# Kernel optimization log

Hardware: AMD Instinct MI355X
Metric: run time of the kernel (lower is better)

Reference implementation:

```python
import jax, jax.numpy as jnp
import numpy as np

ROUTINGS = 3

def squash(s, axis=-1):
    mag_sq = jnp.sum(s * s, axis=axis, keepdims=True)
    mag = jnp.sqrt(mag_sq)
    return mag_sq / (1.0 + mag_sq) * (s / (mag + 1e-8))

def setup_inputs() -> dict:
    key = jax.random.key(0)
    k1, k2 = jax.random.split(key)
    B, I, Din, O, Dout = 256, 1152, 8, 10, 16
    x = jax.random.normal(k1, (B, I, Din), dtype=jnp.float32)
    weight = 0.01 * jax.random.normal(k2, (O, I, Dout, Din), dtype=jnp.float32)
    return {"x": x, "weight": weight}

def reference(x, weight):
    # x: [B, I, Din]; weight: [O, I, Dout, Din]
    # x_hat: [B, O, I, Dout]
    x_hat = jnp.einsum('oidc,bic->boid', weight, x)
    x_hat_det = jax.lax.stop_gradient(x_hat)
    B, O, I, _ = x_hat.shape
    b = jnp.zeros((B, O, I), dtype=x_hat.dtype)
    outputs = None
    for i in range(ROUTINGS):
        c = jax.nn.softmax(b, axis=1)  # softmax over output capsules
        if i == ROUTINGS - 1:
            outputs = squash(jnp.sum(c[:, :, :, None] * x_hat, axis=2, keepdims=True))
        else:
            outputs = squash(jnp.sum(c[:, :, :, None] * x_hat_det, axis=2, keepdims=True))
            b = b + jnp.sum(outputs * x_hat_det, axis=-1)
    return jnp.squeeze(outputs, axis=2)  # [B, O, Dout]
```

## Files before the change

kernel.cpp:

```cpp
#include <hip/hip_runtime.h>

#define BB   256
#define II   1152
#define OO   10
#define DOUT 16
#define NICG 32

using h2 = __fp16 __attribute__((ext_vector_type(2)));
using h4 = __fp16 __attribute__((ext_vector_type(4)));
using h8 = __fp16 __attribute__((ext_vector_type(8)));
#define H2V(v, a, b) __builtin_shufflevector((v), (v), (a), (b))
#define FD(a, b, c)  __builtin_amdgcn_fdot2((a), (b), (c), false)

__device__ __forceinline__ float dpp_add_xor1(float v) {
  int r = __builtin_amdgcn_mov_dpp(__float_as_int(v), 0xB1, 0xF, 0xF, true);
  return v + __int_as_float(r);
}
__device__ __forceinline__ float dpp_add_xor2(float v) {
  int r = __builtin_amdgcn_mov_dpp(__float_as_int(v), 0x4E, 0xF, 0xF, true);
  return v + __int_as_float(r);
}
__device__ __forceinline__ float swz_add_xor4(float v) {
  int r = __builtin_amdgcn_ds_swizzle(__float_as_int(v), 0x101F);
  return v + __int_as_float(r);
}

__device__ __forceinline__ void squash_pair(float v0, float v1,
                                            float& o0, float& o1) {
  float sq = v0 * v0 + v1 * v1;
  sq += __shfl_xor(sq, 1);
  sq += __shfl_xor(sq, 2);
  sq += __shfl_xor(sq, 4);
  const float mag = sqrtf(sq);
  const float t1  = sq / (1.f + sq);
  o0 = t1 * (v0 / (mag + 1e-8f));
  o1 = t1 * (v1 / (mag + 1e-8f));
}

__global__ __launch_bounds__(256) void convert_kernel(
    const float* __restrict__ x, const float* __restrict__ w,
    __fp16* __restrict__ x16, __fp16* __restrict__ w16)
{
  const int bid = blockIdx.x;
  if (bid < 2880) {
    const int t = bid * 256 + threadIdx.x;
    const int e = t & 63;
    const int r = t >> 6;
    const int o = r / II;
    const int i = r - o * II;
    const float2 v2 = *(const float2*)(w + (size_t)r * 128 + e * 2);
    *(h2*)(w16 + ((size_t)i * 12 + o) * 128 + e * 2) =
        __builtin_amdgcn_cvt_pkrtz(v2.x, v2.y);
  } else {
    const size_t t = (size_t)(bid - 2880) * 256 + threadIdx.x;
    const float4 v4 = *(const float4*)(x + t * 4);
    const h2 a = __builtin_amdgcn_cvt_pkrtz(v4.x, v4.y);
    const h2 c = __builtin_amdgcn_cvt_pkrtz(v4.z, v4.w);
    *(h4*)(x16 + t * 4) = __builtin_shufflevector(a, c, 0, 1, 2, 3);
  }
}

template<int K>
__global__ __launch_bounds__(256, 4) void pass_kernel(
    const __fp16* __restrict__ x16,
    const __fp16* __restrict__ w16,
    const float* __restrict__ r0,
    const float* __restrict__ r1,
    float* __restrict__ partial)
{
  const int tid  = threadIdx.x;
  const int lane = tid & 63;
  const int wv   = tid >> 6;
  const int dsub = lane & 7;
  const int bl   = lane >> 3;
  const int icg  = blockIdx.x & 31;
  const int bg   = blockIdx.x >> 5;
  const int b    = bg * 8 + bl;
  const int i0   = (icg * 4 + wv) * 9;

  __shared__ float red[4][8 * 168];

  float Vr[OO][2];
  if (K >= 1) {
#pragma unroll
    for (int o = 0; o < OO; ++o) {
      const float2 a = *(const float2*)(r0 + ((size_t)b * OO + o) * DOUT + dsub * 2);
      float v0, v1;
      squash_pair(a.x, a.y, v0, v1);
      if (K == 2) {
        const float2 c = *(const float2*)(r1 + ((size_t)b * OO + o) * DOUT + dsub * 2);
        float u0, u1;
        squash_pair(c.x, c.y, u0, u1);
        v0 += u0; v1 += u1;
      }
      Vr[o][0] = v0; Vr[o][1] = v1;
    }
  }

  float s[OO][2];
#pragma unroll
  for (int o = 0; o < OO; ++o) { s[o][0] = 0.f; s[o][1] = 0.f; }

  const __fp16* wp = w16 + (size_t)i0 * 1536 + dsub * 16;
  const __fp16* xp = x16 + ((size_t)b * II + i0) * 8;
  h8 xq = *(const h8*)(xp);
  h8 xn = *(const h8*)(xp + 8);

#pragma unroll 1
  for (int ii = 0; ii < 9; ++ii) {
    const h2 xq0 = H2V(xq, 0, 1), xq1 = H2V(xq, 2, 3);
    const h2 xq2 = H2V(xq, 4, 5), xq3 = H2V(xq, 6, 7);

    float xh[OO][2];
    float t[OO];
#pragma unroll
    for (int half = 0; half < 2; ++half) {
      h8 wz[10];
      const __fp16* base = wp + half * 640;
#pragma unroll
      for (int g = 0; g < 5; ++g) {
        wz[2 * g]     = *(const h8*)(base + g * 128);
        wz[2 * g + 1] = *(const h8*)(base + g * 128 + 8);
      }
      __builtin_amdgcn_sched_barrier(0);
#pragma unroll
      for (int g = 0; g < 5; ++g) {
        const int o = half * 5 + g;
        xh[o][0] = FD(H2V(wz[2*g], 0, 1), xq0, FD(H2V(wz[2*g], 2, 3), xq1,
                   FD(H2V(wz[2*g], 4, 5), xq2, FD(H2V(wz[2*g], 6, 7), xq3, 0.f))));
        xh[o][1] = FD(H2V(wz[2*g+1], 0, 1), xq0, FD(H2V(wz[2*g+1], 2, 3), xq1,
                   FD(H2V(wz[2*g+1], 4, 5), xq2, FD(H2V(wz[2*g+1], 6, 7), xq3, 0.f))));
        if (K >= 1)
          t[o] = Vr[o][0] * xh[o][0] + Vr[o][1] * xh[o][1];
      }
    }

    if (K == 0) {
#pragma unroll
      for (int o = 0; o < OO; ++o) { s[o][0] += xh[o][0]; s[o][1] += xh[o][1]; }
    } else {
#pragma unroll
      for (int o = 0; o < OO; ++o) {
        t[o] = dpp_add_xor1(t[o]);
        t[o] = dpp_add_xor2(t[o]);
        t[o] = swz_add_xor4(t[o]);
      }
      float sum = 0.f;
#pragma unroll
      for (int o = 0; o < OO; ++o) { t[o] = __expf(t[o]); sum += t[o]; }
      const float inv = __builtin_amdgcn_rcpf(sum);
#pragma unroll
      for (int o = 0; o < OO; ++o) {
        const float c = t[o] * inv;
        s[o][0] += c * xh[o][0];
        s[o][1] += c * xh[o][1];
      }
    }

    wp += 1536;
    xq = xn;
    const int inx = (ii < 7) ? (i0 + ii + 2) : (i0 + 8);
    xn = *(const h8*)(x16 + ((size_t)b * II + inx) * 8);
  }

  if (K == 0) {
#pragma unroll
    for (int o = 0; o < OO; ++o) { s[o][0] *= 0.1f; s[o][1] *= 0.1f; }
  }

  if (wv != 0) {
    float* rr = red[wv] + bl * 168;
#pragma unroll
    for (int o = 0; o < OO; ++o)
      *(float2*)&rr[o * 16 + dsub * 2] = make_float2(s[o][0], s[o][1]);
  }
  __syncthreads();
  if (wv == 0) {
    float* outp = partial + ((size_t)icg * BB + b) * (OO * DOUT);
#pragma unroll
    for (int o = 0; o < OO; ++o) {
      float a0 = s[o][0], a1 = s[o][1];
#pragma unroll
      for (int r = 1; r < 4; ++r) {
        const float2 v2 = *(const float2*)(red[r] + bl * 168 + o * 16 + dsub * 2);
        a0 += v2.x; a1 += v2.y;
      }
      *(float2*)&outp[o * 16 + dsub * 2] = make_float2(a0, a1);
    }
  }
}

__global__ __launch_bounds__(256) void reduce_plane(
    const float* __restrict__ partial,
    float* __restrict__ plane)
{
  const int idx = blockIdx.x * 256 + threadIdx.x;
  float s = 0.f;
#pragma unroll
  for (int g = 0; g < NICG; ++g)
    s += partial[(size_t)g * (BB * OO * DOUT) + idx];
  plane[idx] = s;
}

__global__ __launch_bounds__(256) void reduce_final(
    const float* __restrict__ partial,
    float* __restrict__ out)
{
  const int idx = blockIdx.x * 256 + threadIdx.x;
  float s = 0.f;
#pragma unroll
  for (int g = 0; g < NICG; ++g)
    s += partial[(size_t)g * (BB * OO * DOUT) + idx];

  float sq = s * s;
  sq += __shfl_xor(sq, 1);
  sq += __shfl_xor(sq, 2);
  sq += __shfl_xor(sq, 4);
  sq += __shfl_xor(sq, 8);
  const float mag = sqrtf(sq);
  out[idx] = sq / (1.f + sq) * (s / (mag + 1e-8f));
}

extern "C" void kernel_launch(void* const* d_in, const int* in_sizes, int n_in,
                              void* d_out, int out_size, void* d_ws, size_t ws_size,
                              hipStream_t stream) {
  const float* x = (const float*)d_in[0];
  const float* w = (const float*)d_in[1];
  float* outp = (float*)d_out;

  const size_t P = (size_t)BB * OO * DOUT;
  float* plane0  = (float*)d_ws;
  float* plane1  = plane0 + P;
  float* partial = plane1 + P;
  __fp16* x16 = (__fp16*)(partial + (size_t)NICG * P);
  __fp16* w16 = x16 + (size_t)BB * II * 8;

  convert_kernel<<<5184, 256, 0, stream>>>(x, w, x16, w16);

  const int pg = 1024;
  const int rg = (int)(P / 256);

  pass_kernel<0><<<pg, 256, 0, stream>>>(x16, w16, nullptr, nullptr, partial);
  reduce_plane<<<rg, 256, 0, stream>>>(partial, plane0);
  pass_kernel<1><<<pg, 256, 0, stream>>>(x16, w16, plane0, nullptr, partial);
  reduce_plane<<<rg, 256, 0, stream>>>(partial, plane1);
  pass_kernel<2><<<pg, 256, 0, stream>>>(x16, w16, plane0, plane1, partial);
  reduce_final<<<rg, 256, 0, stream>>>(partial, outp);
}
```

Before: 157.7 us.

## Software-pipeline weight loads across iterations with register prefetch buffer

Prefetches the first half of the next iteration's weight vectors into registers while the current iteration computes. The second half is loaded at the start of each iteration, so memory latency overlaps with the dot-product and softmax work. The extra 10 h8 registers force lowering launch bounds from 4 to 3 waves-per-SIMD target, trading occupancy for latency hiding.

New measurement: 272.7 us. 1.73x slower.

```diff
diff --git a/kernel.cpp b/kernel.cpp
--- a/kernel.cpp
+++ b/kernel.cpp
@@ -61,7 +61,7 @@
 }
 
 template<int K>
-__global__ __launch_bounds__(256, 4) void pass_kernel(
+__global__ __launch_bounds__(256, 3) void pass_kernel(
     const __fp16* __restrict__ x16,
     const __fp16* __restrict__ w16,
     const float* __restrict__ r0,
@@ -103,6 +103,13 @@
 
   const __fp16* wp = w16 + (size_t)i0 * 1536 + dsub * 16;
   const __fp16* xp = x16 + ((size_t)b * II + i0) * 8;
+
+  h8 pf[10];
+#pragma unroll
+  for (int g = 0; g < 5; ++g) {
+    pf[2 * g]     = *(const h8*)(wp + g * 128);
+    pf[2 * g + 1] = *(const h8*)(wp + g * 128 + 8);
+  }
   h8 xq = *(const h8*)(xp);
   h8 xn = *(const h8*)(xp + 8);
 
@@ -111,28 +118,56 @@
     const h2 xq0 = H2V(xq, 0, 1), xq1 = H2V(xq, 2, 3);
     const h2 xq2 = H2V(xq, 4, 5), xq3 = H2V(xq, 6, 7);
 
+    h8 c0[10];
+#pragma unroll
+    for (int g = 0; g < 10; ++g) c0[g] = pf[g];
+
+    h8 wz[10];
+    {
+      const __fp16* b1 = wp + 640;
+#pragma unroll
+      for (int g = 0; g < 5; ++g) {
+        wz[2 * g]     = *(const h8*)(b1 + g * 128);
+        wz[2 * g + 1] = *(const h8*)(b1 + g * 128 + 8);
+      }
+    }
+    __builtin_amdgcn_sched_barrier(0);
+
+    {
+      const __fp16* wpn = w16 +
+          (size_t)((ii < 8) ? (i0 + ii + 1) : (i0 + 8)) * 1536 + dsub * 16;
+#pragma unroll
+      for (int g = 0; g < 5; ++g) {
+        pf[2 * g]     = *(const h8*)(wpn + g * 128);
+        pf[2 * g + 1] = *(const h8*)(wpn + g * 128 + 8);
+      }
+      xq = xn;
+      const int inx2 = (ii < 7) ? (i0 + ii + 2) : (i0 + 8);
+      xn = *(const h8*)(x16 + ((size_t)b * II + inx2) * 8);
+    }
+    __builtin_amdgcn_sched_barrier(0);
+
     float xh[OO][2];
     float t[OO];
 #pragma unroll
-    for (int half = 0; half < 2; ++half) {
-      h8 wz[10];
-      const __fp16* base = wp + half * 640;
-#pragma unroll
-      for (int g = 0; g < 5; ++g) {
-        wz[2 * g]     = *(const h8*)(base + g * 128);
-        wz[2 * g + 1] = *(const h8*)(base + g * 128 + 8);
-      }
-      __builtin_amdgcn_sched_barrier(0);
-#pragma unroll
-      for (int g = 0; g < 5; ++g) {
-        const int o = half * 5 + g;
-        xh[o][0] = FD(H2V(wz[2*g], 0, 1), xq0, FD(H2V(wz[2*g], 2, 3), xq1,
-                   FD(H2V(wz[2*g], 4, 5), xq2, FD(H2V(wz[2*g], 6, 7), xq3, 0.f))));
-        xh[o][1] = FD(H2V(wz[2*g+1], 0, 1), xq0, FD(H2V(wz[2*g+1], 2, 3), xq1,
-                   FD(H2V(wz[2*g+1], 4, 5), xq2, FD(H2V(wz[2*g+1], 6, 7), xq3, 0.f))));
-        if (K >= 1)
-          t[o] = Vr[o][0] * xh[o][0] + Vr[o][1] * xh[o][1];
-      }
+    for (int g = 0; g < 5; ++g) {
+      const int o = g;
+      xh[o][0] = FD(H2V(c0[2*g], 0, 1), xq0, FD(H2V(c0[2*g], 2, 3), xq1,
+                 FD(H2V(c0[2*g], 4, 5), xq2, FD(H2V(c0[2*g], 6, 7), xq3, 0.f))));
+      xh[o][1] = FD(H2V(c0[2*g+1], 0, 1), xq0, FD(H2V(c0[2*g+1], 2, 3), xq1,
+                 FD(H2V(c0[2*g+1], 4, 5), xq2, FD(H2V(c0[2*g+1], 6, 7), xq3, 0.f))));
+      if (K >= 1)
+        t[o] = Vr[o][0] * xh[o][0] + Vr[o][1] * xh[o][1];
+    }
+#pragma unroll
+    for (int g = 0; g < 5; ++g) {
+      const int o = 5 + g;
+      xh[o][0] = FD(H2V(wz[2*g], 0, 1), xq0, FD(H2V(wz[2*g], 2, 3), xq1,
+                 FD(H2V(wz[2*g], 4, 5), xq2, FD(H2V(wz[2*g], 6, 7), xq3, 0.f))));
+      xh[o][1] = FD(H2V(wz[2*g+1], 0, 1), xq0, FD(H2V(wz[2*g+1], 2, 3), xq1,
+                 FD(H2V(wz[2*g+1], 4, 5), xq2, FD(H2V(wz[2*g+1], 6, 7), xq3, 0.f))));
+      if (K >= 1)
+        t[o] = Vr[o][0] * xh[o][0] + Vr[o][1] * xh[o][1];
     }
 
     if (K == 0) {
@@ -158,9 +193,6 @@
     }
 
     wp += 1536;
-    xq = xn;
-    const int inx = (ii < 7) ? (i0 + ii + 2) : (i0 + 8);
-    xn = *(const h8*)(x16 + ((size_t)b * II + inx) * 8);
   }
 
   if (K == 0) {
```

## Software-pipeline weight loads across iterations with double-buffered registers

Applied to the files above, without the earlier changes.

The pass kernel now prefetches the first half of the next iteration's weights into a ping-pong register buffer while computing the current one, and loads the second half of the current weights before the barrier. The loop is unrolled by two to alternate buffers. Launch bounds drop from 4 to 2 blocks per CU to leave room for the extra registers. The aim is to hide global load latency, at the cost of lower occupancy and more register pressure.

After: 174.5 us. +10.7%, slower.

```diff
diff --git a/kernel.cpp b/kernel.cpp
--- a/kernel.cpp
+++ b/kernel.cpp
@@ -61,7 +61,7 @@
 }
 
 template<int K>
-__global__ __launch_bounds__(256, 4) void pass_kernel(
+__global__ __launch_bounds__(256, 2) void pass_kernel(
     const __fp16* __restrict__ x16,
     const __fp16* __restrict__ w16,
     const float* __restrict__ r0,
@@ -101,67 +101,94 @@
 #pragma unroll
   for (int o = 0; o < OO; ++o) { s[o][0] = 0.f; s[o][1] = 0.f; }
 
-  const __fp16* wp = w16 + (size_t)i0 * 1536 + dsub * 16;
   const __fp16* xp = x16 + ((size_t)b * II + i0) * 8;
+  const __fp16* wbase = w16 + dsub * 16;
+
+  h8 pfA[10], pfB[10], wz[10];
+
+#pragma unroll
+  for (int g = 0; g < 5; ++g) {
+    const __fp16* p = wbase + (size_t)i0 * 1536 + g * 128;
+    pfA[2 * g]     = *(const h8*)(p);
+    pfA[2 * g + 1] = *(const h8*)(p + 8);
+  }
   h8 xq = *(const h8*)(xp);
   h8 xn = *(const h8*)(xp + 8);
 
+  #define BODY(CUR, NXT, II_)                                                   \
+  {                                                                             \
+    const int i = i0 + (II_);                                                   \
+    const h2 xq0 = H2V(xq, 0, 1), xq1 = H2V(xq, 2, 3);                          \
+    const h2 xq2 = H2V(xq, 4, 5), xq3 = H2V(xq, 6, 7);                          \
+    const __fp16* wrow = wbase + (size_t)i * 1536;                              \
+    _Pragma("unroll")                                                           \
+    for (int g = 0; g < 5; ++g) {                              \
+      wz[2 * g]     = *(const h8*)(wrow + 640 + g * 128);                       \
+      wz[2 * g + 1] = *(const h8*)(wrow + 640 + g * 128 + 8);                   \
+    }                                                                           \
+    {                                            \
+      const int in1 = ((II_) < 8) ? (i0 + (II_) + 1) : (i0 + 8);                \
+      const __fp16* wnx = wbase + (size_t)in1 * 1536;                           \
+      _Pragma("unroll")                                                         \
+      for (int g = 0; g < 5; ++g) {                                             \
+        NXT[2 * g]     = *(const h8*)(wnx + g * 128);                           \
+        NXT[2 * g + 1] = *(const h8*)(wnx + g * 128 + 8);                       \
+      }                                                                         \
+      xq = xn;                                                                  \
+      const int in2 = ((II_) < 7) ? (i0 + (II_) + 2) : (i0 + 8);                \
+      xn = *(const h8*)(x16 + ((size_t)b * II + in2) * 8);                      \
+    }                                                                           \
+    __builtin_amdgcn_sched_barrier(0);            \
+    float xh[OO][2];                                                            \
+    float t[OO];                                                                \
+    _Pragma("unroll")                                                           \
+    for (int g = 0; g < 5; ++g) {            \
+      xh[g][0] = FD(H2V(CUR[2*g], 0, 1), xq0, FD(H2V(CUR[2*g], 2, 3), xq1,      \
+                 FD(H2V(CUR[2*g], 4, 5), xq2, FD(H2V(CUR[2*g], 6, 7), xq3, 0.f))));\
+      xh[g][1] = FD(H2V(CUR[2*g+1], 0, 1), xq0, FD(H2V(CUR[2*g+1], 2, 3), xq1,  \
+                 FD(H2V(CUR[2*g+1], 4, 5), xq2, FD(H2V(CUR[2*g+1], 6, 7), xq3, 0.f))));\
+      if (K >= 1) t[g] = Vr[g][0] * xh[g][0] + Vr[g][1] * xh[g][1];             \
+    }                                                                           \
+    _Pragma("unroll")                                                           \
+    for (int g = 0; g < 5; ++g) {                            \
+      const int o = 5 + g;                                                      \
+      xh[o][0] = FD(H2V(wz[2*g], 0, 1), xq0, FD(H2V(wz[2*g], 2, 3), xq1,        \
+                 FD(H2V(wz[2*g], 4, 5), xq2, FD(H2V(wz[2*g], 6, 7), xq3, 0.f))));\
+      xh[o][1] = FD(H2V(wz[2*g+1], 0, 1), xq0, FD(H2V(wz[2*g+1], 2, 3), xq1,    \
+                 FD(H2V(wz[2*g+1], 4, 5), xq2, FD(H2V(wz[2*g+1], 6, 7), xq3, 0.f))));\
+      if (K >= 1) t[o] = Vr[o][0] * xh[o][0] + Vr[o][1] * xh[o][1];             \
+    }                                                                           \
+    if (K == 0) {                                                               \
+      _Pragma("unroll")                                                         \
+      for (int o = 0; o < OO; ++o) { s[o][0] += xh[o][0]; s[o][1] += xh[o][1]; }\
+    } else {                                                                    \
+      _Pragma("unroll")                                                         \
+      for (int o = 0; o < OO; ++o) {                                            \
+        t[o] = dpp_add_xor1(t[o]);                                              \
+        t[o] = dpp_add_xor2(t[o]);                                              \
+        t[o] = swz_add_xor4(t[o]);                                              \
+      }                                                                         \
+      float sum = 0.f;                                                          \
+      _Pragma("unroll")                                                         \
+      for (int o = 0; o < OO; ++o) { t[o] = __expf(t[o]); sum += t[o]; }        \
+      const float inv = __builtin_amdgcn_rcpf(sum);                             \
+      _Pragma("unroll")                                                         \
+      for (int o = 0; o < OO; ++o) {                                            \
+        const float c = t[o] * inv;                                             \
+        s[o][0] += c * xh[o][0];                                                \
+        s[o][1] += c * xh[o][1];                                                \
+      }                                                                         \
+    }                                                                           \
+  }
+
 #pragma unroll 1
-  for (int ii = 0; ii < 9; ++ii) {
-    const h2 xq0 = H2V(xq, 0, 1), xq1 = H2V(xq, 2, 3);
-    const h2 xq2 = H2V(xq, 4, 5), xq3 = H2V(xq, 6, 7);
-
-    float xh[OO][2];
-    float t[OO];
-#pragma unroll
-    for (int half = 0; half < 2; ++half) {
-      h8 wz[10];
-      const __fp16* base = wp + half * 640;
-#pragma unroll
-      for (int g = 0; g < 5; ++g) {
-        wz[2 * g]     = *(const h8*)(base + g * 128);
-        wz[2 * g + 1] = *(const h8*)(base + g * 128 + 8);
-      }
-      __builtin_amdgcn_sched_barrier(0);
-#pragma unroll
-      for (int g = 0; g < 5; ++g) {
-        const int o = half * 5 + g;
-        xh[o][0] = FD(H2V(wz[2*g], 0, 1), xq0, FD(H2V(wz[2*g], 2, 3), xq1,
-                   FD(H2V(wz[2*g], 4, 5), xq2, FD(H2V(wz[2*g], 6, 7), xq3, 0.f))));
-        xh[o][1] = FD(H2V(wz[2*g+1], 0, 1), xq0, FD(H2V(wz[2*g+1], 2, 3), xq1,
-                   FD(H2V(wz[2*g+1], 4, 5), xq2, FD(H2V(wz[2*g+1], 6, 7), xq3, 0.f))));
-        if (K >= 1)
-          t[o] = Vr[o][0] * xh[o][0] + Vr[o][1] * xh[o][1];
-      }
-    }
-
-    if (K == 0) {
-#pragma unroll
-      for (int o = 0; o < OO; ++o) { s[o][0] += xh[o][0]; s[o][1] += xh[o][1]; }
-    } else {
-#pragma unroll
-      for (int o = 0; o < OO; ++o) {
-        t[o] = dpp_add_xor1(t[o]);
-        t[o] = dpp_add_xor2(t[o]);
-        t[o] = swz_add_xor4(t[o]);
-      }
-      float sum = 0.f;
-#pragma unroll
-      for (int o = 0; o < OO; ++o) { t[o] = __expf(t[o]); sum += t[o]; }
-      const float inv = __builtin_amdgcn_rcpf(sum);
-#pragma unroll
-      for (int o = 0; o < OO; ++o) {
-        const float c = t[o] * inv;
-        s[o][0] += c * xh[o][0];
-        s[o][1] += c * xh[o][1];
-      }
-    }
-
-    wp += 1536;
-    xq = xn;
-    const int inx = (ii < 7) ? (i0 + ii + 2) : (i0 + 8);
-    xn = *(const h8*)(x16 + ((size_t)b * II + inx) * 8);
-  }
+  for (int p = 0; p < 4; ++p) {
+    const int ii = p * 2;
+    BODY(pfA, pfB, ii)
+    BODY(pfB, pfA, ii + 1)
+  }
+  BODY(pfA, pfB, 8)
+  #undef BODY
 
   if (K == 0) {
 #pragma unroll
```
